# Optimization experiments

Measured on AMD Instinct MI355X. Metric: run time of the kernel, lower is better.

The kernel has to match this reference:

```python
import jax, jax.numpy as jnp
import numpy as np

WIRES = 24
DIMS = [2] * WIRES
INDEX = [0, 2, 3, 4, 5, 6, 7, 8, 9, 10, 11]  # control = wire 0, targets = wires 2..11
D_CONTROL = DIMS[INDEX[0]]                   # 2
D_TARGET = int(np.prod([DIMS[i] for i in INDEX[1:]]))  # 1024
REMAINING = [i for i in range(WIRES) if i not in INDEX]
D_REM = int(np.prod([DIMS[i] for i in REMAINING])) if REMAINING else 1  # 8192
NEW_ORDER = INDEX + REMAINING
INV_ORDER = [NEW_ORDER.index(i) for i in range(WIRES)]
N = int(np.prod(DIMS))  # 2**24


def setup_inputs() -> dict:
    key = jax.random.key(0)
    k1, k2, k3, k4 = jax.random.split(key, 4)
    return {
        "x_real": jax.random.normal(k1, (N,), dtype=jnp.float32),
        "x_imag": jax.random.normal(k2, (N,), dtype=jnp.float32),
        "U_real": jax.random.normal(k3, (D_CONTROL, D_TARGET, D_TARGET), dtype=jnp.float32),
        "U_imag": jax.random.normal(k4, (D_CONTROL, D_TARGET, D_TARGET), dtype=jnp.float32),
    }


def reference(x_real, x_imag, U_real, U_imag):
    x = (x_real + 1j * x_imag).astype(jnp.complex64)
    A = (U_real + 1j * U_imag).astype(jnp.complex64)  # [d_c, d_t, d_t]
    # Skew-Hermitian generator -> unitary blocks via batched matrix exponential
    skew = A - jnp.conj(jnp.swapaxes(A, -1, -2))
    U_blocks = jax.vmap(jax.scipy.linalg.expm)(skew)  # [d_c, d_t, d_t]

    # Bring control + target wires to the front
    st = x.reshape(DIMS).transpose(NEW_ORDER)          # [2]*wires permuted
    A_blk = st.reshape(D_CONTROL, D_TARGET, D_REM)     # [d_c, d_t, d_rem]

    # Block-diagonal unitary applied as a batched per-control matmul
    out = jnp.einsum('ktd,kdr->ktr', U_blocks, A_blk)  # [d_c, d_t, d_rem]

    new_shape = ([D_CONTROL] + [DIMS[i] for i in INDEX[1:]]
                 + ([DIMS[i] for i in REMAINING] if REMAINING else []))
    state_new = out.reshape(new_shape).transpose(INV_ORDER).reshape(-1, 1)
    # Return as stacked (real, imag) float32 since the state is complex64
    return jnp.stack([state_new.real, state_new.imag])  # [2, N, 1]
```

## Files before the change

### kernel.cpp

```cpp
#include <hip/hip_runtime.h>
#include <hip/hip_bf16.h>

#define PLANE (1 << 20)

typedef __attribute__((ext_vector_type(8))) short bf16x8;
typedef __attribute__((ext_vector_type(4))) float f32x4;

struct SegOff { long o[6]; };

union U4 { ushort u[4]; unsigned long long v; };

__device__ __forceinline__ ushort bf16bits(float v) {
    union { __hip_bfloat16 b; ushort u; } c;
    c.b = __float2bfloat16(v);
    return c.u;
}

__device__ __forceinline__ void split2(float v, ushort& hi, ushort& lo) {
    union { __hip_bfloat16 b; ushort u; } c;
    __hip_bfloat16 h = __float2bfloat16(v);
    c.b = h; hi = c.u;
    c.b = __float2bfloat16(v - __bfloat162float(h));
    lo = c.u;
}

__device__ __forceinline__ void gload16(const ushort* g, ushort* l) {
    __builtin_amdgcn_global_load_lds(
        (const __attribute__((address_space(1))) unsigned int*)g,
        (__attribute__((address_space(3))) unsigned int*)l, 16, 0, 0);
}

__global__ __launch_bounds__(256) void build_skew_k(
    const float* __restrict__ Ure, const float* __restrict__ Uim,
    float* __restrict__ Bre, float* __restrict__ Bim, float scale)
{
    int idx = blockIdx.x * 256 + threadIdx.x;
    int ij  = idx & (PLANE - 1);
    int i   = ij >> 10, j = ij & 1023;
    int t   = (idx & ~(PLANE - 1)) | (j << 10) | i;
    Bre[idx] = (Ure[idx] - Ure[t]) * scale;
    Bim[idx] = (Uim[idx] + Uim[t]) * scale;
}

__global__ __launch_bounds__(256) void init_T_k(
    const float* __restrict__ Bre, const float* __restrict__ Bim,
    float* __restrict__ Tre, float* __restrict__ Tim, float inv)
{
    int idx = blockIdx.x * 256 + threadIdx.x;
    int ij  = idx & (PLANE - 1);
    int i   = ij >> 10, j = ij & 1023;
    Tre[idx] = Bre[idx] * inv + ((i == j) ? 1.0f : 0.0f);
    Tim[idx] = Bim[idx] * inv;
}

__global__ __launch_bounds__(256) void reduce_k(
    float* __restrict__ C, const float* __restrict__ PB, float scale, int addI)
{
    long e = ((long)blockIdx.x * 256 + threadIdx.x) * 4;
    float4 v = *(float4*)(C + e);
    const float4 a = *(const float4*)(PB + e);
    const float4 b = *(const float4*)(PB + 4L * PLANE + e);
    const float4 c = *(const float4*)(PB + 8L * PLANE + e);
    v.x = (v.x + a.x + b.x + c.x) * scale;
    v.y = (v.y + a.y + b.y + c.y) * scale;
    v.z = (v.z + a.z + b.z + c.z) * scale;
    v.w = (v.w + a.w + b.w + c.w) * scale;
    if (addI) {
        long p = e >> 20;
        if (p < 2) {
            int ij = (int)(e & (PLANE - 1));
            int i = ij >> 10, j = ij & 1023;
            if (i >= j && i < j + 4) ((float*)&v)[i - j] += 1.0f;
        }
    }
    *(float4*)(C + e) = v;
}

__global__ __launch_bounds__(256) void pack_A6_k(
    const float* __restrict__ Sre, const float* __restrict__ Sim,
    ushort* __restrict__ Ab)
{
    int idx = blockIdx.x * 256 + threadIdx.x;
    int k   = idx >> 18;
    int m   = (idx >> 8) & 1023;
    int c4  = (idx & 255) * 4;
    const float4 vr = *(const float4*)(Sre + (size_t)k * PLANE + (size_t)m * 1024 + c4);
    const float4 vi = *(const float4*)(Sim + (size_t)k * PLANE + (size_t)m * 1024 + c4);
    U4 rh, rl, ih, il, nih, nil;
    split2(vr.x, rh.u[0], rl.u[0]); split2(vr.y, rh.u[1], rl.u[1]);
    split2(vr.z, rh.u[2], rl.u[2]); split2(vr.w, rh.u[3], rl.u[3]);
    split2(vi.x, ih.u[0], il.u[0]); split2(vi.y, ih.u[1], il.u[1]);
    split2(vi.z, ih.u[2], il.u[2]); split2(vi.w, ih.u[3], il.u[3]);
    #pragma unroll
    for (int i = 0; i < 4; ++i) { nih.u[i] = ih.u[i] ^ 0x8000; nil.u[i] = il.u[i] ^ 0x8000; }

    long b0 = (long)k * 1024 * 6144 + (long)m * 6144;
    long b1 = (long)(2 + k) * 1024 * 6144 + (long)m * 6144;
    *(unsigned long long*)&Ab[b0 + 0*1024 + c4] = rh.v;
    *(unsigned long long*)&Ab[b0 + 1*1024 + c4] = rh.v;
    *(unsigned long long*)&Ab[b0 + 2*1024 + c4] = rl.v;
    *(unsigned long long*)&Ab[b0 + 3*1024 + c4] = nih.v;
    *(unsigned long long*)&Ab[b0 + 4*1024 + c4] = nih.v;
    *(unsigned long long*)&Ab[b0 + 5*1024 + c4] = nil.v;
    *(unsigned long long*)&Ab[b1 + 0*1024 + c4] = ih.v;
    *(unsigned long long*)&Ab[b1 + 1*1024 + c4] = ih.v;
    *(unsigned long long*)&Ab[b1 + 2*1024 + c4] = il.v;
    *(unsigned long long*)&Ab[b1 + 3*1024 + c4] = rh.v;
    *(unsigned long long*)&Ab[b1 + 4*1024 + c4] = rh.v;
    *(unsigned long long*)&Ab[b1 + 5*1024 + c4] = rl.v;
}

__global__ __launch_bounds__(256) void pack_A4_k(
    const float* __restrict__ Sre, const float* __restrict__ Sim,
    ushort* __restrict__ Ab)
{
    int idx = blockIdx.x * 256 + threadIdx.x;
    int k   = idx >> 18;
    int m   = (idx >> 8) & 1023;
    int c4  = (idx & 255) * 4;
    const float4 vr = *(const float4*)(Sre + (size_t)k * PLANE + (size_t)m * 1024 + c4);
    const float4 vi = *(const float4*)(Sim + (size_t)k * PLANE + (size_t)m * 1024 + c4);
    U4 rh, rl, ih, il, nih, nil;
    split2(vr.x, rh.u[0], rl.u[0]); split2(vr.y, rh.u[1], rl.u[1]);
    split2(vr.z, rh.u[2], rl.u[2]); split2(vr.w, rh.u[3], rl.u[3]);
    split2(vi.x, ih.u[0], il.u[0]); split2(vi.y, ih.u[1], il.u[1]);
    split2(vi.z, ih.u[2], il.u[2]); split2(vi.w, ih.u[3], il.u[3]);
    #pragma unroll
    for (int i = 0; i < 4; ++i) { nih.u[i] = ih.u[i] ^ 0x8000; nil.u[i] = il.u[i] ^ 0x8000; }

    long b0 = (long)k * 1024 * 4096 + (long)m * 4096;
    long b1 = (long)(2 + k) * 1024 * 4096 + (long)m * 4096;
    *(unsigned long long*)&Ab[b0 + 0*1024 + c4] = rh.v;
    *(unsigned long long*)&Ab[b0 + 1*1024 + c4] = rl.v;
    *(unsigned long long*)&Ab[b0 + 2*1024 + c4] = nih.v;
    *(unsigned long long*)&Ab[b0 + 3*1024 + c4] = nil.v;
    *(unsigned long long*)&Ab[b1 + 0*1024 + c4] = ih.v;
    *(unsigned long long*)&Ab[b1 + 1*1024 + c4] = il.v;
    *(unsigned long long*)&Ab[b1 + 2*1024 + c4] = rh.v;
    *(unsigned long long*)&Ab[b1 + 3*1024 + c4] = rl.v;
}

__global__ __launch_bounds__(256) void pack_BT6_k(
    const float* __restrict__ Sre, const float* __restrict__ Sim,
    ushort* __restrict__ Tt)
{
    __shared__ float Lre[64][65];
    __shared__ float Lim[64][65];
    int k = blockIdx.z, r0 = blockIdx.y * 64, c0 = blockIdx.x * 64;
    int tid = threadIdx.x;
    const float* br = Sre + (size_t)k * PLANE;
    const float* bi = Sim + (size_t)k * PLANE;
    #pragma unroll
    for (int p = 0; p < 16; ++p) {
        int idx = p * 256 + tid, r = idx >> 6, c = idx & 63;
        Lre[r][c] = br[(size_t)(r0 + r) * 1024 + c0 + c];
        Lim[r][c] = bi[(size_t)(r0 + r) * 1024 + c0 + c];
    }
    __syncthreads();
    #pragma unroll
    for (int p = 0; p < 4; ++p) {
        int s = p * 256 + tid, oc = s >> 4, r4 = (s & 15) * 4;
        U4 rh, rl, ih, il;
        #pragma unroll
        for (int i = 0; i < 4; ++i) {
            split2(Lre[r4 + i][oc], rh.u[i], rl.u[i]);
            split2(Lim[r4 + i][oc], ih.u[i], il.u[i]);
        }
        size_t dst = (size_t)k * PLANE + (size_t)(c0 + oc) * 1024 + r0 + r4;
        *(unsigned long long*)&Tt[0L * 2 * PLANE + dst] = rh.v;
        *(unsigned long long*)&Tt[1L * 2 * PLANE + dst] = rl.v;
        *(unsigned long long*)&Tt[2L * 2 * PLANE + dst] = ih.v;
        *(unsigned long long*)&Tt[3L * 2 * PLANE + dst] = il.v;
    }
}

__global__ __launch_bounds__(256) void pack_xT_k(
    const float* __restrict__ xre, const float* __restrict__ xim,
    ushort* __restrict__ xT)
{
    __shared__ float Lre[64][65];
    __shared__ float Lim[64][65];
    int pl = blockIdx.z, t0 = blockIdx.y * 64, c0 = blockIdx.x * 64;
    int tid = threadIdx.x;
    const float* br = xre + ((size_t)pl << 22);
    const float* bi = xim + ((size_t)pl << 22);
    #pragma unroll
    for (int p = 0; p < 16; ++p) {
        int idx = p * 256 + tid, r = idx >> 6, c = idx & 63;
        Lre[r][c] = br[(size_t)(t0 + r) * 4096 + c0 + c];
        Lim[r][c] = bi[(size_t)(t0 + r) * 4096 + c0 + c];
    }
    __syncthreads();
    #pragma unroll
    for (int p = 0; p < 4; ++p) {
        int s = p * 256 + tid, oc = s >> 4, r4 = (s & 15) * 4;
        U4 re4, im4;
        #pragma unroll
        for (int i = 0; i < 4; ++i) {
            re4.u[i] = bf16bits(Lre[r4 + i][oc]);
            im4.u[i] = bf16bits(Lim[r4 + i][oc]);
        }
        size_t dst = ((size_t)pl << 22) + (size_t)(c0 + oc) * 1024 + t0 + r4;
        *(unsigned long long*)&xT[dst] = re4.v;
        *(unsigned long long*)&xT[(4L << 22) + dst] = im4.v;
    }
}

__global__ __launch_bounds__(256, 2) void gemm_bt_k(
    const ushort* __restrict__ Ab, long aPackStride, long aInnerStride, int aInnerDiv, int aLd,
    const ushort* __restrict__ Bb, SegOff segs, long bZStride,
    float* __restrict__ CreB, float* __restrict__ CimB, long cZStride, int cLd,
    int kLen, int zHalf, float scale, int addI,
    float* __restrict__ PB)
{
    __shared__ ushort As[128 * 32];
    __shared__ ushort Bs[128 * 32];

    const int zTot  = 2 * zHalf;
    const int chunk = blockIdx.z / zTot;
    const int zb    = blockIdx.z % zTot;
    const int pack = zb / zHalf, inner = zb % zHalf;
    const ushort* A = Ab + (long)pack * aPackStride + (long)(inner / aInnerDiv) * aInnerStride;
    float* C = (chunk == 0)
        ? ((pack ? CimB : CreB) + (long)inner * cZStride)
        : (PB + (long)(chunk - 1) * 4 * PLANE + (long)pack * 2 * PLANE + (long)inner * PLANE);

    const int tid = threadIdx.x;
    const int lane = tid & 63, wave = tid >> 6;
    const int m0 = blockIdx.y * 128, n0 = blockIdx.x * 128;
    const int wm = (wave >> 1) * 64, wn = (wave & 1) * 64;
    const int l15 = lane & 15, quad = lane >> 4;

    f32x4 acc[4][4] = {};

    const int kStart = chunk * kLen, kEnd = kStart + kLen;
    for (int kb = kStart; kb < kEnd; kb += 32) {
        const ushort* Bp = Bb + segs.o[kb >> 10] + (long)inner * bZStride + (kb & 1023);
        #pragma unroll
        for (int q = 0; q < 2; ++q) {
            int c = q * 256 + wave * 64 + lane;
            gload16(A + (long)(m0 + (c >> 2)) * aLd + kb + (c & 3) * 8,
                    &As[(q * 256 + wave * 64) * 8]);
            gload16(Bp + (long)(n0 + (c >> 2)) * 1024 + (c & 3) * 8,
                    &Bs[(q * 256 + wave * 64) * 8]);
        }
        __syncthreads();
        bf16x8 af[4], bfr[4];
        #pragma unroll
        for (int i = 0; i < 4; ++i)
            af[i] = *(const bf16x8*)&As[(wm + i * 16 + l15) * 32 + quad * 8];
        #pragma unroll
        for (int j = 0; j < 4; ++j)
            bfr[j] = *(const bf16x8*)&Bs[(wn + j * 16 + l15) * 32 + quad * 8];
        #pragma unroll
        for (int i = 0; i < 4; ++i)
            #pragma unroll
            for (int j = 0; j < 4; ++j)
                acc[i][j] = __builtin_amdgcn_mfma_f32_16x16x32_bf16(af[i], bfr[j], acc[i][j], 0, 0, 0);
        __syncthreads();
    }

    #pragma unroll
    for (int i = 0; i < 4; ++i) {
        int row0 = m0 + wm + i * 16 + quad * 4;
        #pragma unroll
        for (int j = 0; j < 4; ++j) {
            int col = n0 + wn + j * 16 + l15;
            #pragma unroll
            for (int r = 0; r < 4; ++r) {
                float v = acc[i][j][r] * scale;
                if (addI && chunk == 0 && pack == 0 && (row0 + r) == col) v += 1.0f;
                C[(long)(row0 + r) * cLd + col] = v;
            }
        }
    }
}

extern "C" void kernel_launch(void* const* d_in, const int* in_sizes, int n_in,
                              void* d_out, int out_size, void* d_ws, size_t ws_size,
                              hipStream_t stream)
{
    const float* x_re = (const float*)d_in[0];
    const float* x_im = (const float*)d_in[1];
    const float* U_re = (const float*)d_in[2];
    const float* U_im = (const float*)d_in[3];
    float* out = (float*)d_out;

    float* fp = (float*)d_ws;
    float* Tre = fp + 0L * 2 * PLANE;
    float* Tim = fp + 1L * 2 * PLANE;
    float* Rre = fp + 2L * 2 * PLANE;
    float* Rim = fp + 3L * 2 * PLANE;
    float* BSre = fp + 4L * 2 * PLANE;
    float* BSim = fp + 5L * 2 * PLANE;
    ushort* Askew = (ushort*)((char*)d_ws + (48L << 20));
    ushort* At    = (ushort*)((char*)d_ws + (96L << 20));
    ushort* Tt    = (ushort*)((char*)d_ws + (144L << 20));
    ushort* Aap   = Askew;
    ushort* xT    = At;
    float* Phorner = (float*)At;
    float* Psquare = (float*)Askew;

    dim3 blk(256);

    const float scaleB = 1.0f / 512.0f;
    build_skew_k<<<dim3(2 * PLANE / 256), blk, 0, stream>>>(U_re, U_im, BSre, BSim, scaleB);
    init_T_k<<<dim3(2 * PLANE / 256), blk, 0, stream>>>(BSre, BSim, Tre, Tim, 1.0f / 8.0f);
    pack_A6_k<<<dim3(2048), blk, 0, stream>>>(BSre, BSim, Askew);

    SegOff se;
    se.o[0] = 0L;           se.o[1] = 2L * PLANE;  se.o[2] = 0L;
    se.o[3] = 4L * PLANE;   se.o[4] = 6L * PLANE;  se.o[5] = 4L * PLANE;

    dim3 ge(8, 8, 16);
    dim3 gr(PLANE / 256);
    for (int j = 7; j >= 1; --j) {
        pack_BT6_k<<<dim3(16, 16, 2), blk, 0, stream>>>(Tre, Tim, Tt);
        gemm_bt_k<<<ge, blk, 0, stream>>>(Askew, 2L * 1024 * 6144, 1024L * 6144, 1, 6144,
                                          Tt, se, (long)PLANE,
                                          Rre, Rim, (long)PLANE, 1024,
                                          1536, 2, 1.0f, 0, Phorner);
        reduce_k<<<gr, blk, 0, stream>>>(Rre, Phorner, 1.0f / (float)j, 1);
        float* t;
        t = Tre; Tre = Rre; Rre = t;
        t = Tim; Tim = Rim; Rim = t;
    }
    for (int s = 0; s < 9; ++s) {
        pack_A6_k<<<dim3(2048), blk, 0, stream>>>(Tre, Tim, At);
        pack_BT6_k<<<dim3(16, 16, 2), blk, 0, stream>>>(Tre, Tim, Tt);
        gemm_bt_k<<<ge, blk, 0, stream>>>(At, 2L * 1024 * 6144, 1024L * 6144, 1, 6144,
                                          Tt, se, (long)PLANE,
                                          Rre, Rim, (long)PLANE, 1024,
                                          1536, 2, 1.0f, 0, Psquare);
        reduce_k<<<gr, blk, 0, stream>>>(Rre, Psquare, 1.0f, 0);
        float* t;
        t = Tre; Tre = Rre; Rre = t;
        t = Tim; Tim = Rim; Rim = t;
    }

    pack_A4_k<<<dim3(2048), blk, 0, stream>>>(Tre, Tim, Aap);
    pack_xT_k<<<dim3(64, 16, 4), blk, 0, stream>>>(x_re, x_im, xT);

    SegOff sa;
    sa.o[0] = 0L;        sa.o[1] = 0L;
    sa.o[2] = 4L << 22;  sa.o[3] = 4L << 22;
    sa.o[4] = 0L;        sa.o[5] = 0L;

    gemm_bt_k<<<dim3(32, 8, 8), blk, 0, stream>>>(Aap, 2L * 1024 * 4096, 1024L * 4096, 2, 4096,
                                                  xT, sa, 1L << 22,
                                                  out, out + (1L << 24), 1L << 22, 4096,
                                                  4096, 4, 1.0f, 0, (float*)nullptr);
}
```

Baseline: 2.421 ms.

## Replace 128x128 GEMM with 256x256 double-buffered, swizzled, 8-wave GEMM kernel

Replaces the 128x128 tile, 4-wave, single-buffered bf16 MFMA GEMM with a 256x256 tile, 8-wave kernel that uses a K-step of 64. Global loads go into double-buffered LDS through an XOR swizzle, with waitcnt-based prefetch two stages ahead, and MFMA phases are interleaved with s_barrier and setprio. The goal is higher arithmetic intensity per LDS/global byte, hiding load latency, and avoiding LDS bank conflicts. In exchange it uses 128KB of LDS and more accumulator registers, and the grid gets smaller (256 blocks for the expm GEMMs), which may reduce occupancy and CU utilisation.

```diff
diff --git a/kernel.cpp b/kernel.cpp
--- a/kernel.cpp
+++ b/kernel.cpp
@@ -206,69 +206,109 @@
     }
 }
 
-__global__ __launch_bounds__(256, 2) void gemm_bt_k(
+__global__ __launch_bounds__(512, 2) void gemm256_k(
     const ushort* __restrict__ Ab, long aPackStride, long aInnerStride, int aInnerDiv, int aLd,
     const ushort* __restrict__ Bb, SegOff segs, long bZStride,
     float* __restrict__ CreB, float* __restrict__ CimB, long cZStride, int cLd,
     int kLen, int zHalf, float scale, int addI,
     float* __restrict__ PB)
 {
-    __shared__ ushort As[128 * 32];
-    __shared__ ushort Bs[128 * 32];
+    __shared__ ushort lds[2][32768];
 
     const int zTot  = 2 * zHalf;
     const int chunk = blockIdx.z / zTot;
     const int zb    = blockIdx.z % zTot;
-    const int pack = zb / zHalf, inner = zb % zHalf;
+    const int pack  = zb / zHalf, inner = zb % zHalf;
     const ushort* A = Ab + (long)pack * aPackStride + (long)(inner / aInnerDiv) * aInnerStride;
     float* C = (chunk == 0)
         ? ((pack ? CimB : CreB) + (long)inner * cZStride)
         : (PB + (long)(chunk - 1) * 4 * PLANE + (long)pack * 2 * PLANE + (long)inner * PLANE);
 
-    const int tid = threadIdx.x;
+    const int tid  = threadIdx.x;
     const int lane = tid & 63, wave = tid >> 6;
-    const int m0 = blockIdx.y * 128, n0 = blockIdx.x * 128;
-    const int wm = (wave >> 1) * 64, wn = (wave & 1) * 64;
+    const int wr = wave >> 2, wc = wave & 3;
     const int l15 = lane & 15, quad = lane >> 4;
-
-    f32x4 acc[4][4] = {};
-
-    const int kStart = chunk * kLen, kEnd = kStart + kLen;
-    for (int kb = kStart; kb < kEnd; kb += 32) {
-        const ushort* Bp = Bb + segs.o[kb >> 10] + (long)inner * bZStride + (kb & 1023);
+    const int m0 = blockIdx.y * 256, n0 = blockIdx.x * 256;
+
+    const int srow  = lane >> 3;
+    const int scolE = ((((lane & 7) * 16) ^ (((lane >> 5) & 1) << 5)) >> 1);
+    const int xorv  = ((l15 >> 2) & 1) << 5;
+    const int abase = ((((wr * 128 + l15) * 128 + quad * 16) ^ xorv) >> 1);
+    const int bbase = ((((wc * 64  + l15) * 128 + quad * 16) ^ xorv) >> 1);
+
+    const int kStart = chunk * kLen;
+    const int nt = kLen >> 6;
+
+    f32x4 acc[8][4] = {};
+
+#define STAGE(T, BUF)                                                          \
+    {                                                                          \
+        int kb_ = kStart + (T) * 64;                                           \
+        const ushort* Ag_ = A + (long)m0 * aLd + kb_;                          \
+        const ushort* Bg_ = Bb + segs.o[kb_ >> 10] + (long)inner * bZStride    \
+                            + (long)n0 * 1024 + (kb_ & 1023);                  \
+        ushort* lA_ = &lds[BUF][0];                                            \
+        ushort* lB_ = &lds[BUF][16384];                                        \
+        _Pragma("unroll")                                                      \
+        for (int i_ = 0; i_ < 4; ++i_) {                                       \
+            int br_ = (wave * 4 + i_) * 8 + srow;                              \
+            gload16(Ag_ + (long)br_ * aLd + scolE, lA_ + (wave * 4 + i_) * 512); \
+            gload16(Bg_ + (long)br_ * 1024 + scolE, lB_ + (wave * 4 + i_) * 512); \
+        }                                                                      \
+    }
+
+#define PHASE(MQ, KQ, LOADB)                                                   \
+    {                                                                          \
+        if (LOADB) {                                                           \
+            _Pragma("unroll")                                                  \
+            for (int j_ = 0; j_ < 4; ++j_)                                     \
+                bfr[j_] = *(const bf16x8*)&lB[bbase + j_ * 1024 + (KQ) * 32];  \
+        }                                                                      \
+        bf16x8 aa[4];                                                          \
+        _Pragma("unroll")                                                      \
+        for (int i_ = 0; i_ < 4; ++i_)                                         \
+            aa[i_] = *(const bf16x8*)&lA[abase + ((MQ) * 4 + i_) * 1024 + (KQ) * 32]; \
+        asm volatile("s_barrier" ::: "memory");                                \
+        __builtin_amdgcn_s_setprio(1);                                         \
+        _Pragma("unroll")                                                      \
+        for (int i_ = 0; i_ < 4; ++i_) {                                       \
+            _Pragma("unroll")                                                  \
+            for (int j_ = 0; j_ < 4; ++j_)                                     \
+                acc[(MQ) * 4 + i_][j_] = __builtin_amdgcn_mfma_f32_16x16x32_bf16( \
+                    aa[i_], bfr[j_], acc[(MQ) * 4 + i_][j_], 0, 0, 0);         \
+        }                                                                      \
+        __builtin_amdgcn_s_setprio(0);                                         \
+        asm volatile("s_barrier" ::: "memory");                                \
+    }
+
+    STAGE(0, 0);
+    STAGE(1, 1);
+
+    for (int t = 0; t < nt; ++t) {
+        ushort* lA = &lds[t & 1][0];
+        ushort* lB = &lds[t & 1][16384];
+        if (t + 1 < nt) { asm volatile("s_waitcnt vmcnt(8)" ::: "memory"); }
+        else            { asm volatile("s_waitcnt vmcnt(0)" ::: "memory"); }
+        asm volatile("s_barrier" ::: "memory");
+        bf16x8 bfr[4];
+        PHASE(0, 0, 1);
+        PHASE(1, 0, 0);
+        PHASE(0, 1, 1);
+        PHASE(1, 1, 0);
+        if (t + 2 < nt) STAGE(t + 2, t & 1);
+    }
+#undef PHASE
+#undef STAGE
+
+    #pragma unroll
+    for (int fm = 0; fm < 8; ++fm) {
+        int row0 = m0 + wr * 128 + fm * 16 + quad * 4;
         #pragma unroll
-        for (int q = 0; q < 2; ++q) {
-            int c = q * 256 + wave * 64 + lane;
-            gload16(A + (long)(m0 + (c >> 2)) * aLd + kb + (c & 3) * 8,
-                    &As[(q * 256 + wave * 64) * 8]);
-            gload16(Bp + (long)(n0 + (c >> 2)) * 1024 + (c & 3) * 8,
-                    &Bs[(q * 256 + wave * 64) * 8]);
-        }
-        __syncthreads();
-        bf16x8 af[4], bfr[4];
-        #pragma unroll
-        for (int i = 0; i < 4; ++i)
-            af[i] = *(const bf16x8*)&As[(wm + i * 16 + l15) * 32 + quad * 8];
-        #pragma unroll
-        for (int j = 0; j < 4; ++j)
-            bfr[j] = *(const bf16x8*)&Bs[(wn + j * 16 + l15) * 32 + quad * 8];
-        #pragma unroll
-        for (int i = 0; i < 4; ++i)
-            #pragma unroll
-            for (int j = 0; j < 4; ++j)
-                acc[i][j] = __builtin_amdgcn_mfma_f32_16x16x32_bf16(af[i], bfr[j], acc[i][j], 0, 0, 0);
-        __syncthreads();
-    }
-
-    #pragma unroll
-    for (int i = 0; i < 4; ++i) {
-        int row0 = m0 + wm + i * 16 + quad * 4;
-        #pragma unroll
-        for (int j = 0; j < 4; ++j) {
-            int col = n0 + wn + j * 16 + l15;
+        for (int fn = 0; fn < 4; ++fn) {
+            int col = n0 + wc * 64 + fn * 16 + l15;
             #pragma unroll
             for (int r = 0; r < 4; ++r) {
-                float v = acc[i][j][r] * scale;
+                float v = acc[fm][fn][r] * scale;
                 if (addI && chunk == 0 && pack == 0 && (row0 + r) == col) v += 1.0f;
                 C[(long)(row0 + r) * cLd + col] = v;
             }
@@ -302,6 +342,7 @@
     float* Psquare = (float*)Askew;
 
     dim3 blk(256);
+    dim3 blk5(512);
 
     const float scaleB = 1.0f / 512.0f;
     build_skew_k<<<dim3(2 * PLANE / 256), blk, 0, stream>>>(U_re, U_im, BSre, BSim, scaleB);
@@ -312,14 +353,14 @@
     se.o[0] = 0L;           se.o[1] = 2L * PLANE;  se.o[2] = 0L;
     se.o[3] = 4L * PLANE;   se.o[4] = 6L * PLANE;  se.o[5] = 4L * PLANE;
 
-    dim3 ge(8, 8, 16);
+    dim3 ge(4, 4, 16);
     dim3 gr(PLANE / 256);
     for (int j = 7; j >= 1; --j) {
         pack_BT6_k<<<dim3(16, 16, 2), blk, 0, stream>>>(Tre, Tim, Tt);
-        gemm_bt_k<<<ge, blk, 0, stream>>>(Askew, 2L * 1024 * 6144, 1024L * 6144, 1, 6144,
-                                          Tt, se, (long)PLANE,
-                                          Rre, Rim, (long)PLANE, 1024,
-                                          1536, 2, 1.0f, 0, Phorner);
+        gemm256_k<<<ge, blk5, 0, stream>>>(Askew, 2L * 1024 * 6144, 1024L * 6144, 1, 6144,
+                                           Tt, se, (long)PLANE,
+                                           Rre, Rim, (long)PLANE, 1024,
+                                           1536, 2, 1.0f, 0, Phorner);
         reduce_k<<<gr, blk, 0, stream>>>(Rre, Phorner, 1.0f / (float)j, 1);
         float* t;
         t = Tre; Tre = Rre; Rre = t;
@@ -328,10 +369,10 @@
     for (int s = 0; s < 9; ++s) {
         pack_A6_k<<<dim3(2048), blk, 0, stream>>>(Tre, Tim, At);
         pack_BT6_k<<<dim3(16, 16, 2), blk, 0, stream>>>(Tre, Tim, Tt);
-        gemm_bt_k<<<ge, blk, 0, stream>>>(At, 2L * 1024 * 6144, 1024L * 6144, 1, 6144,
-                                          Tt, se, (long)PLANE,
-                                          Rre, Rim, (long)PLANE, 1024,
-                                          1536, 2, 1.0f, 0, Psquare);
+        gemm256_k<<<ge, blk5, 0, stream>>>(At, 2L * 1024 * 6144, 1024L * 6144, 1, 6144,
+                                           Tt, se, (long)PLANE,
+                                           Rre, Rim, (long)PLANE, 1024,
+                                           1536, 2, 1.0f, 0, Psquare);
         reduce_k<<<gr, blk, 0, stream>>>(Rre, Psquare, 1.0f, 0);
         float* t;
         t = Tre; Tre = Rre; Rre = t;
@@ -346,8 +387,8 @@
     sa.o[2] = 4L << 22;  sa.o[3] = 4L << 22;
     sa.o[4] = 0L;        sa.o[5] = 0L;
 
-    gemm_bt_k<<<dim3(32, 8, 8), blk, 0, stream>>>(Aap, 2L * 1024 * 4096, 1024L * 4096, 2, 4096,
-                                                  xT, sa, 1L << 22,
-                                                  out, out + (1L << 24), 1L << 22, 4096,
-                                                  4096, 4, 1.0f, 0, (float*)nullptr);
-}
+    gemm256_k<<<dim3(16, 4, 8), blk5, 0, stream>>>(Aap, 2L * 1024 * 4096, 1024L * 4096, 2, 4096,
+                                                   xT, sa, 1L << 22,
+                                                   out, out + (1L << 24), 1L << 22, 4096,
+                                                   4096, 4, 1.0f, 0, (float*)nullptr);
+}
```

New measurement: 2.246 ms. 7.2% less time.
